# Kernel tuning notes

Measured on AMD Instinct MI355X. Metric: run time of the kernel, lower is better.

Reference implementation:

```python
import jax, jax.numpy as jnp
import numpy as np

B, S, D, H, NS = 4, 2048, 1024, 16, 300
DK = D // H                      # 64
NSP = (NS + H - 1) // H * H      # 304 (padded skills)
DG = NSP // H                    # 19
NEG_FILL = -1e9                  # fp32 path in the torch module


def setup_inputs() -> dict:
    key = jax.random.key(0)
    ks = jax.random.split(key, 12)
    sc = 0.02
    return {
        "context_sequence": jax.random.normal(ks[0], (B, S, D), jnp.float32),
        "value_sequence": jax.random.normal(ks[1], (B, S, NS), jnp.float32),
        "mask": jnp.triu(jnp.ones((S, S), jnp.bool_), k=1),  # causal: True = masked
        # weights stored as [in, out] (math-equivalent to torch's x @ W.T + b)
        "Wq": jax.random.normal(ks[2], (D, D), jnp.float32) * sc,
        "bq": jnp.zeros((D,), jnp.float32),
        "Wk": jax.random.normal(ks[3], (D, D), jnp.float32) * sc,
        "bk": jnp.zeros((D,), jnp.float32),
        "Wv": jax.random.normal(ks[4], (NS, NS), jnp.float32) * sc,
        "bv": jnp.zeros((NS,), jnp.float32),
        "Wg": jax.random.normal(ks[5], (NS, D), jnp.float32) * sc,  # gain_to_context
        "bg": jnp.zeros((D,), jnp.float32),
        "Wo": jax.random.normal(ks[6], (D, D), jnp.float32) * sc,   # output_proj
        "bo": jnp.zeros((D,), jnp.float32),
    }


def reference(context_sequence, value_sequence, mask,
              Wq, bq, Wk, bk, Wv, bv, Wg, bg, Wo, bo):
    b = context_sequence.shape[0]
    orig_dtype = context_sequence.dtype

    # Q, K: [b, H, S, DK]
    Q = (context_sequence @ Wq + bq).reshape(b, -1, H, DK).transpose(0, 2, 1, 3)
    K = (context_sequence @ Wk + bk).reshape(b, -1, H, DK).transpose(0, 2, 1, 3)

    # intrinsic-gain V: project in skill space, zero-pad to NSP, split heads -> [b, H, S, DG]
    V_proj = value_sequence @ Wv + bv
    V_proj = jnp.pad(V_proj, ((0, 0), (0, 0), (0, NSP - NS)))
    V = V_proj.reshape(b, -1, H, DG).transpose(0, 2, 1, 3)

    # fp32 score upcast, scale by sqrt(d_k), mask, cast back, softmax
    scores = jnp.einsum('bhqd,bhkd->bhqk',
                        Q.astype(jnp.float32), K.astype(jnp.float32)) / np.sqrt(DK)
    scores = jnp.where(mask, NEG_FILL, scores).astype(orig_dtype)
    attn = jax.nn.softmax(scores, axis=-1)

    # [b, H, S, DG] -> [b, S, NSP] -> slice to NS
    head_gains = jnp.einsum('bhqk,bhkd->bhqd', attn, V)
    agg = head_gains.transpose(0, 2, 1, 3).reshape(b, -1, NSP)[..., :NS]

    output = agg @ Wg + bg            # gain_to_context
    return output @ Wo + bo           # output_proj (dropout is identity in eval)
```

## Files before the change

### kernel.cpp

```cpp
#include <hip/hip_runtime.h>
#include <math.h>

#define B_   4
#define S_   2048
#define D_   1024
#define H_   16
#define DK_  64
#define NS_  300
#define NSP_ 304
#define DG_  19
#define M_   (B_ * S_)

typedef short bf16x8 __attribute__((ext_vector_type(8)));
typedef short s16x8  __attribute__((ext_vector_type(8)));
typedef short s16x4  __attribute__((ext_vector_type(4)));
typedef float f32x4  __attribute__((ext_vector_type(4)));

__device__ __forceinline__ short f2bf(float f) {
    unsigned u = __float_as_uint(f);
    u += 0x7FFFu + ((u >> 16) & 1u);
    return (short)(u >> 16);
}
__device__ __forceinline__ s16x4 f2bf4(float4 v) {
    s16x4 s; s[0] = f2bf(v.x); s[1] = f2bf(v.y); s[2] = f2bf(v.z); s[3] = f2bf(v.w);
    return s;
}
__device__ __forceinline__ float bf2f(short s) {
    return __uint_as_float(((unsigned)(unsigned short)s) << 16);
}

__device__ __forceinline__ void gload16(const void* g, void* l) {
    __builtin_amdgcn_global_load_lds(
        (const __attribute__((address_space(1))) unsigned int*)g,
        (__attribute__((address_space(3))) unsigned int*)l, 16, 0, 0);
}

__global__ __launch_bounds__(256) void pack_x(const float* __restrict__ src,
                                              short* __restrict__ dst) {
    const int total = M_ * (D_ / 8);
    for (int i = blockIdx.x * 256 + threadIdx.x; i < total; i += gridDim.x * 256) {
        const float4 a = *(const float4*)(src + (size_t)i * 8);
        const float4 b = *(const float4*)(src + (size_t)i * 8 + 4);
        s16x8 o;
        o[0]=f2bf(a.x); o[1]=f2bf(a.y); o[2]=f2bf(a.z); o[3]=f2bf(a.w);
        o[4]=f2bf(b.x); o[5]=f2bf(b.y); o[6]=f2bf(b.z); o[7]=f2bf(b.w);
        *(s16x8*)(dst + (size_t)i * 8) = o;
    }
}

__global__ __launch_bounds__(256) void pack_v(const float* __restrict__ src,
                                              short* __restrict__ dst) {
    const int total = M_ * 75;
    for (int i = blockIdx.x * 256 + threadIdx.x; i < total; i += gridDim.x * 256) {
        const int row = i / 75, c4 = (i - row * 75) * 4;
        const float4 v = *(const float4*)(src + (size_t)row * NS_ + c4);
        *(s16x4*)(dst + (size_t)row * 320 + c4) = f2bf4(v);
    }
}

__global__ __launch_bounds__(256) void transpack_all(
    const float* __restrict__ Wq, const float* __restrict__ Wk,
    const float* __restrict__ Wv, const float* __restrict__ Wo,
    short* __restrict__ WqkT, short* __restrict__ WvT, short* __restrict__ WoT)
{
    __shared__ float tsh[64][65];
    const int z = blockIdx.z, bx = blockIdx.x, by = blockIdx.y;
    const float* src; short* dst; int srs, KR, drs; float scale = 1.f;
    if (z == 0)      { src = Wq; dst = WqkT;              srs = D_;  KR = D_;  drs = D_;  scale = 0.125f; }
    else if (z == 1) { src = Wk; dst = WqkT + 1024 * D_;  srs = D_;  KR = D_;  drs = D_; }
    else if (z == 2) { if (bx >= 5 || by >= 6) return;
                       src = Wv; dst = WvT;               srs = NS_; KR = NS_; drs = 320; }
    else             { src = Wo; dst = WoT;               srs = D_;  KR = D_;  drs = D_; }

    const int k0 = bx * 64, n0 = by * 64;
    const int tt = threadIdx.x;
    const int nx = tt & 63, kyb = tt >> 6;
#pragma unroll
    for (int j = 0; j < 16; ++j) {
        const int k = kyb + j * 4;
        float v = 0.f;
        if (k0 + k < KR && n0 + nx < KR) v = src[(size_t)(k0 + k) * srs + n0 + nx];
        tsh[nx][k] = v;
    }
    __syncthreads();
    const int kx = tt & 63, nyb = tt >> 6;
#pragma unroll
    for (int j = 0; j < 16; ++j) {
        const int n = nyb + j * 4;
        dst[(size_t)(n0 + n) * drs + k0 + kx] = f2bf(tsh[n][kx] * scale);
    }
}

__global__ __launch_bounds__(256) void pack_misc(
    const float* __restrict__ bq, const float* __restrict__ bk, float* __restrict__ bqk,
    short* __restrict__ VpT,
    const float* __restrict__ Wg, short* __restrict__ Wgb)
{
    const int bid = blockIdx.x, t = threadIdx.x;
    if (bid < 8) {
        const int i = bid * 256 + t;
        if (i < 1024) bqk[i] = bq[i] * 0.125f;
        else bqk[i] = bk[i - 1024];
    } else if (bid < 72) {
        const int bh = bid - 8;
        short* row = VpT + ((size_t)bh * 20 + 19) * 2048;
        *(s16x8*)(row + t * 8) = (s16x8)0;
    } else {
        const int i = (bid - 72) * 256 + t;
        const int r = i >> 8, c4 = (i & 255) * 4;
        float4 v = make_float4(0.f, 0.f, 0.f, 0.f);
        if (r < NS_) v = *(const float4*)(Wg + (size_t)r * D_ + c4);
        *(s16x4*)(Wgb + (size_t)r * D_ + c4) = f2bf4(v);
    }
}

__global__ __launch_bounds__(256) void pack_bfused2(const short* __restrict__ WoT,
                                                    const float* __restrict__ bg,
                                                    const float* __restrict__ bo,
                                                    float* __restrict__ dst) {
    __shared__ float part[4];
    const int n = blockIdx.x, t = threadIdx.x;
    const s16x4 w = *(const s16x4*)(WoT + (size_t)n * D_ + t * 4);
    const float4 bgv = *(const float4*)(bg + t * 4);
    float acc = bf2f(w[0]) * bgv.x + bf2f(w[1]) * bgv.y
              + bf2f(w[2]) * bgv.z + bf2f(w[3]) * bgv.w;
#pragma unroll
    for (int m = 1; m < 64; m <<= 1) acc += __shfl_xor(acc, m);
    if ((t & 63) == 0) part[t >> 6] = acc;
    __syncthreads();
    if (t == 0) dst[n] = bo[n] + ((part[0] + part[1]) + (part[2] + part[3]));
}

template<int MODE>
__global__ __launch_bounds__(256) void gemm_k(
    const short* __restrict__ A, int lda,
    const short* __restrict__ Bt, int ldb,
    const float* __restrict__ bias, int blen,
    void* __restrict__ C, int ldc, int nzero, int nstore,
    int K, int gx)
{
    __shared__ __align__(16) short smem[(MODE == 1) ? 17408 : 16384];
    short* As = smem;
    short* Bs = smem + 8192;

    const int nwg = gridDim.x, q = nwg >> 3, fid = blockIdx.x;
    const int wg = (fid & 7) * q + (fid >> 3);
    const int bn = wg % gx, bm = wg / gx;

    const int t = threadIdx.x, l = t & 63, w = t >> 6;
    const int wm = w >> 1, wn = w & 1;
    const int g = l >> 4, c = l & 15;
    const int fsw = (c & 7) << 4;

    const int so  = l * 16;
    const int srow = so >> 7;
    const int skb  = (so & 127) ^ ((srow & 7) << 4);

    f32x4 acc[4][4] = {};
    const size_t ldab = (size_t)lda * 2, ldbb = (size_t)ldb * 2;
    const char* Ab = (const char*)A + (size_t)(bm * 128) * ldab;
    const char* Bb = (const char*)Bt + (size_t)(bn * 128) * ldbb;

    for (int k0 = 0; k0 < K; k0 += 64) {
#pragma unroll
        for (int i = 0; i < 4; ++i) {
            const int chunk = w * 4 + i;
            const int row = chunk * 8 + srow;
            gload16(Ab + (size_t)row * ldab + (size_t)(k0 * 2) + skb,
                    (char*)As + chunk * 1024);
            gload16(Bb + (size_t)row * ldbb + (size_t)(k0 * 2) + skb,
                    (char*)Bs + chunk * 1024);
        }
        __syncthreads();

#pragma unroll
        for (int ks = 0; ks < 2; ++ks) {
            const int kb = (ks * 64 + g * 16) ^ fsw;
            bf16x8 af[4], bf[4];
#pragma unroll
            for (int mt = 0; mt < 4; ++mt)
                af[mt] = *(const bf16x8*)((const char*)As + (wm * 64 + mt * 16 + c) * 128 + kb);
#pragma unroll
            for (int nt = 0; nt < 4; ++nt)
                bf[nt] = *(const bf16x8*)((const char*)Bs + (wn * 64 + nt * 16 + c) * 128 + kb);
            __builtin_amdgcn_s_setprio(1);
#pragma unroll
            for (int mt = 0; mt < 4; ++mt)
#pragma unroll
                for (int nt = 0; nt < 4; ++nt)
                    acc[mt][nt] = __builtin_amdgcn_mfma_f32_16x16x32_bf16(
                        af[mt], bf[nt], acc[mt][nt], 0, 0, 0);
            __builtin_amdgcn_s_setprio(0);
        }
        __syncthreads();
    }

    if (MODE == 1) {
        short* Cs = smem;
#pragma unroll
        for (int mt = 0; mt < 4; ++mt) {
#pragma unroll
            for (int nt = 0; nt < 4; ++nt) {
                const int coll = wn * 64 + nt * 16 + c;
                const int colg = bn * 128 + coll;
                const float bb = (colg < blen) ? bias[colg] : 0.f;
#pragma unroll
                for (int r = 0; r < 4; ++r) {
                    const int rowl = wm * 64 + mt * 16 + 4 * g + r;
                    const short v = (colg < nzero) ? f2bf(acc[mt][nt][r] + bb) : (short)0;
                    Cs[rowl * 136 + coll] = v;
                }
            }
        }
        __syncthreads();
        const int rowl = t >> 1, half = t & 1;
        const int rowg = bm * 128 + rowl;
        short* Cb = (short*)C;
#pragma unroll
        for (int j = 0; j < 8; ++j) {
            const int colg = bn * 128 + half * 64 + j * 8;
            if (colg < nstore)
                *(s16x8*)(Cb + (size_t)rowg * ldc + colg) =
                    *(const s16x8*)(Cs + rowl * 136 + half * 64 + j * 8);
        }
        return;
    }

#pragma unroll
    for (int mt = 0; mt < 4; ++mt) {
#pragma unroll
        for (int nt = 0; nt < 4; ++nt) {
            const int col = bn * 128 + wn * 64 + nt * 16 + c;
            if (MODE == 2) {
                if (col < NSP_) {
                    const int hh = col / DG_, dg = col - hh * DG_;
                    const float bb = (col < blen) ? bias[col] : 0.f;
                    const int m0 = bm * 128 + wm * 64 + mt * 16 + 4 * g;
                    const int bb_ = m0 >> 11, s = m0 & 2047;
                    s16x4 v;
#pragma unroll
                    for (int r = 0; r < 4; ++r) v[r] = f2bf(acc[mt][nt][r] + bb);
                    *(s16x4*)((short*)C + ((size_t)(bb_ * 16 + hh) * 20 + dg) * 2048 + s) = v;
                }
            } else if (col < nstore) {
                const float bb = (col < blen) ? bias[col] : 0.f;
#pragma unroll
                for (int r = 0; r < 4; ++r) {
                    const int row = bm * 128 + wm * 64 + mt * 16 + 4 * g + r;
                    ((float*)C)[(size_t)row * ldc + col] = acc[mt][nt][r] + bb;
                }
            }
        }
    }
}

__global__ __launch_bounds__(256) void attn2(
    const short* __restrict__ QKb, const short* __restrict__ VpT,
    short* __restrict__ aggP)
{
    __shared__ __align__(16) short Qs[64 * 64];
    __shared__ __align__(16) short Ks[128 * 64];
    __shared__ __align__(16) short Vt[32 * 128];
    __shared__ __align__(16) short Pl[4][16 * 128];

    const int fid = blockIdx.x;
    const int wg = (fid & 7) * 256 + (fid >> 3);
    const int b = wg >> 9, h = (wg >> 5) & 15, qt = 31 - (wg & 31);
    const int q0 = qt * 64;

    const int t = threadIdx.x, l = t & 63, w = t >> 6;
    const int g = l >> 4, c = l & 15;
    const int fsw = (c & 7) << 4;

    const char* QKc = (const char*)QKb;
    const char* Vc  = (const char*)VpT + ((size_t)(b * 16 + h) * 20) * 4096;

#pragma unroll
    for (int i = 0; i < 2; ++i) {
        const int chunk = w * 2 + i;
        const int o = chunk * 1024 + l * 16;
        const int row = o >> 7;
        const int kb = (o & 127) ^ ((row & 7) << 4);
        gload16(QKc + (size_t)(b * S_ + q0 + row) * 4096 + h * 128 + kb,
                (char*)Qs + chunk * 1024);
    }
    if (t < 192) *(s16x8*)((char*)Vt + 5120 + t * 16) = (s16x8)0;
    __syncthreads();

    bf16x8 aq[2];
#pragma unroll
    for (int ks = 0; ks < 2; ++ks)
        aq[ks] = *(const bf16x8*)((const char*)Qs + (w * 16 + c) * 128 + ((ks * 64 + g * 16) ^ fsw));

    float l_run[4];
    f32x4 oacc[2] = {};
#pragma unroll
    for (int r = 0; r < 4; ++r) l_run[r] = 0.f;

    const int nkt = (qt >> 1) + 1;
    for (int kt = 0; kt < nkt; ++kt) {
        const int k0 = kt * 128;
#pragma unroll
        for (int i = 0; i < 4; ++i) {
            const int chunk = w * 4 + i;
            const int o = chunk * 1024 + l * 16;
            const int row = o >> 7;
            const int kb = (o & 127) ^ ((row & 7) << 4);
            gload16(QKc + (size_t)(b * S_ + k0 + row) * 4096 + 2048 + h * 128 + kb,
                    (char*)Ks + chunk * 1024);
        }
        for (int i = w; i < 5; i += 4) {
            const int o = i * 1024 + l * 16;
            const int row = o >> 8;
            const int kb = (o & 255) ^ ((row & 7) << 4);
            gload16(Vc + (size_t)row * 4096 + (size_t)(k0 * 2) + kb,
                    (char*)Vt + i * 1024);
        }
        __syncthreads();

        f32x4 st[8] = {};
        __builtin_amdgcn_s_setprio(1);
#pragma unroll
        for (int ks = 0; ks < 2; ++ks) {
            const int kb = (ks * 64 + g * 16) ^ fsw;
#pragma unroll
            for (int nt = 0; nt < 8; ++nt) {
                const bf16x8 bk = *(const bf16x8*)((const char*)Ks + (nt * 16 + c) * 128 + kb);
                st[nt] = __builtin_amdgcn_mfma_f32_16x16x32_bf16(aq[ks], bk, st[nt], 0, 0, 0);
            }
        }
        __builtin_amdgcn_s_setprio(0);

        if (kt == nkt - 1) {
#pragma unroll
            for (int nt = 0; nt < 8; ++nt) {
                const int kvg = k0 + nt * 16 + c;
#pragma unroll
                for (int r = 0; r < 4; ++r) {
                    const int qg = q0 + w * 16 + 4 * g + r;
                    if (kvg > qg) st[nt][r] = -INFINITY;
                }
            }
        }

#pragma unroll
        for (int nt = 0; nt < 8; ++nt)
#pragma unroll
            for (int r = 0; r < 4; ++r)
                st[nt][r] = __expf(st[nt][r]);
#pragma unroll
        for (int r = 0; r < 4; ++r)
            l_run[r] += ((st[0][r] + st[1][r]) + (st[2][r] + st[3][r]))
                      + ((st[4][r] + st[5][r]) + (st[6][r] + st[7][r]));

#pragma unroll
        for (int nt = 0; nt < 8; ++nt)
#pragma unroll
            for (int r = 0; r < 4; ++r)
                Pl[w][(4 * g + r) * 128 + ((nt * 16 + c) ^ (g << 4))] = f2bf(st[nt][r]);

        __builtin_amdgcn_s_setprio(1);
#pragma unroll
        for (int ks = 0; ks < 4; ++ks) {
            const bf16x8 ap = *(const bf16x8*)((const char*)&Pl[w][0] +
                ((c * 256 + ks * 64 + g * 16) ^ (((c >> 2) & 3) << 5)));
            const int kb = (ks * 64 + g * 16) ^ fsw;
#pragma unroll
            for (int nt = 0; nt < 2; ++nt) {
                const bf16x8 bv = *(const bf16x8*)((const char*)Vt + (nt * 16 + c) * 256 + kb);
                oacc[nt] = __builtin_amdgcn_mfma_f32_16x16x32_bf16(ap, bv, oacc[nt], 0, 0, 0);
            }
        }
        __builtin_amdgcn_s_setprio(0);
        __syncthreads();
    }

    float inv[4];
#pragma unroll
    for (int r = 0; r < 4; ++r) {
        float ls = l_run[r];
        ls += __shfl_xor(ls, 1);
        ls += __shfl_xor(ls, 2);
        ls += __shfl_xor(ls, 4);
        ls += __shfl_xor(ls, 8);
        inv[r] = 1.f / ls;
    }
#pragma unroll
    for (int nt = 0; nt < 2; ++nt) {
        const int dg = nt * 16 + c;
        if (dg < DG_) {
#pragma unroll
            for (int r = 0; r < 4; ++r) {
                const int qg = q0 + w * 16 + 4 * g + r;
                aggP[(size_t)(b * S_ + qg) * 320 + h * DG_ + dg] = f2bf(oacc[nt][r] * inv[r]);
            }
        }
    }
}

extern "C" void kernel_launch(void* const* d_in, const int* in_sizes, int n_in,
                              void* d_out, int out_size, void* d_ws, size_t ws_size,
                              hipStream_t stream)
{
    const float* X    = (const float*)d_in[0];
    const float* Vseq = (const float*)d_in[1];
    const float* Wq = (const float*)d_in[3];
    const float* bq = (const float*)d_in[4];
    const float* Wk = (const float*)d_in[5];
    const float* bk = (const float*)d_in[6];
    const float* Wv = (const float*)d_in[7];
    const float* bv = (const float*)d_in[8];
    const float* Wg = (const float*)d_in[9];
    const float* bg = (const float*)d_in[10];
    const float* Wo = (const float*)d_in[11];
    const float* bo = (const float*)d_in[12];
    float* out = (float*)d_out;

    char* p = (char*)d_ws;
    short* Xb    = (short*)p; p += (size_t)M_ * D_ * 2;
    short* QKb   = (short*)p; p += (size_t)M_ * 2048 * 2;
    short* Xv    = (short*)p; p += (size_t)M_ * 320 * 2;
    short* VpT   = (short*)p; p += (size_t)64 * 20 * 2048 * 2;
    short* aggP  = (short*)p; p += (size_t)M_ * 320 * 2;
    short* WqkT  = (short*)p; p += (size_t)2048 * 1024 * 2;
    short* WvT   = (short*)p; p += (size_t)384 * 320 * 2;
    short* Wgb   = (short*)p; p += (size_t)384 * 1024 * 2;
    short* WoT   = (short*)p; p += (size_t)1024 * 1024 * 2;
    short* WgWoT = (short*)p; p += (size_t)1024 * 320 * 2;
    float* bqk   = (float*)p; p += 2048 * 4;
    float* bfus  = (float*)p; p += 1024 * 4;

    pack_x<<<2048, 256, 0, stream>>>(X, Xb);
    pack_v<<<2400, 256, 0, stream>>>(Vseq, Xv);
    transpack_all<<<dim3(16, 16, 4), 256, 0, stream>>>(Wq, Wk, Wv, Wo, WqkT, WvT, WoT);
    pack_misc<<<456, 256, 0, stream>>>(bq, bk, bqk, VpT, Wg, Wgb);
    pack_bfused2<<<D_, 256, 0, stream>>>(WoT, bg, bo, bfus);

    gemm_k<1><<<16 * 64, 256, 0, stream>>>(Xb, D_, WqkT, D_, bqk, 2048,
                                           QKb, 2048, 2048, 2048, D_, 16);
    gemm_k<2><<<3 * 64, 256, 0, stream>>>(Xv, 320, WvT, 320, bv, NS_,
                                          VpT, 0, 0, 0, 320, 3);
    gemm_k<1><<<3 * 8, 256, 0, stream>>>(WoT, D_, Wgb, D_, bfus, 0,
                                         WgWoT, 320, NS_, 320, D_, 3);
    attn2<<<2048, 256, 0, stream>>>(QKb, VpT, aggP);
    gemm_k<0><<<8 * 64, 256, 0, stream>>>(aggP, 320, WgWoT, 320, bfus, D_,
                                          out, D_, D_, D_, 320, 8);
}
```

Baseline: 323.5 us.

## Merge pack and GEMM launches into mega-kernels, stage final GEMM stores through LDS

Folds the five packing kernels into one megapack launch, with the fused bias now computed from the fp32 Wo instead of a separate pass over packed WoT. It also folds the three independent GEMMs into one megagemm launch that branches on block index. The final fp32 GEMM now stages its output tile through LDS for coalesced float4 stores, and the attention P buffer switches from XOR swizzle to a padded row stride. The aim is to cut launch overhead and tail gaps between small kernels and to improve store coalescing, at the cost of heterogeneous blocks sharing one kernel's resources.

After: 300.9 us. -7.0%, faster.

```diff
diff --git a/kernel.cpp b/kernel.cpp
--- a/kernel.cpp
+++ b/kernel.cpp
@@ -25,9 +25,6 @@
     s16x4 s; s[0] = f2bf(v.x); s[1] = f2bf(v.y); s[2] = f2bf(v.z); s[3] = f2bf(v.w);
     return s;
 }
-__device__ __forceinline__ float bf2f(short s) {
-    return __uint_as_float(((unsigned)(unsigned short)s) << 16);
-}
 
 __device__ __forceinline__ void gload16(const void* g, void* l) {
     __builtin_amdgcn_global_load_lds(
@@ -35,116 +32,111 @@
         (__attribute__((address_space(3))) unsigned int*)l, 16, 0, 0);
 }
 
-__global__ __launch_bounds__(256) void pack_x(const float* __restrict__ src,
-                                              short* __restrict__ dst) {
-    const int total = M_ * (D_ / 8);
-    for (int i = blockIdx.x * 256 + threadIdx.x; i < total; i += gridDim.x * 256) {
-        const float4 a = *(const float4*)(src + (size_t)i * 8);
-        const float4 b = *(const float4*)(src + (size_t)i * 8 + 4);
-        s16x8 o;
-        o[0]=f2bf(a.x); o[1]=f2bf(a.y); o[2]=f2bf(a.z); o[3]=f2bf(a.w);
-        o[4]=f2bf(b.x); o[5]=f2bf(b.y); o[6]=f2bf(b.z); o[7]=f2bf(b.w);
-        *(s16x8*)(dst + (size_t)i * 8) = o;
-    }
-}
-
-__global__ __launch_bounds__(256) void pack_v(const float* __restrict__ src,
-                                              short* __restrict__ dst) {
-    const int total = M_ * 75;
-    for (int i = blockIdx.x * 256 + threadIdx.x; i < total; i += gridDim.x * 256) {
-        const int row = i / 75, c4 = (i - row * 75) * 4;
-        const float4 v = *(const float4*)(src + (size_t)row * NS_ + c4);
-        *(s16x4*)(dst + (size_t)row * 320 + c4) = f2bf4(v);
-    }
-}
-
-__global__ __launch_bounds__(256) void transpack_all(
+__global__ __launch_bounds__(256) void megapack(
+    const float* __restrict__ X, const float* __restrict__ Vseq,
     const float* __restrict__ Wq, const float* __restrict__ Wk,
     const float* __restrict__ Wv, const float* __restrict__ Wo,
-    short* __restrict__ WqkT, short* __restrict__ WvT, short* __restrict__ WoT)
-{
-    __shared__ float tsh[64][65];
-    const int z = blockIdx.z, bx = blockIdx.x, by = blockIdx.y;
-    const float* src; short* dst; int srs, KR, drs; float scale = 1.f;
-    if (z == 0)      { src = Wq; dst = WqkT;              srs = D_;  KR = D_;  drs = D_;  scale = 0.125f; }
-    else if (z == 1) { src = Wk; dst = WqkT + 1024 * D_;  srs = D_;  KR = D_;  drs = D_; }
-    else if (z == 2) { if (bx >= 5 || by >= 6) return;
-                       src = Wv; dst = WvT;               srs = NS_; KR = NS_; drs = 320; }
-    else             { src = Wo; dst = WoT;               srs = D_;  KR = D_;  drs = D_; }
-
-    const int k0 = bx * 64, n0 = by * 64;
-    const int tt = threadIdx.x;
-    const int nx = tt & 63, kyb = tt >> 6;
-#pragma unroll
-    for (int j = 0; j < 16; ++j) {
-        const int k = kyb + j * 4;
-        float v = 0.f;
-        if (k0 + k < KR && n0 + nx < KR) v = src[(size_t)(k0 + k) * srs + n0 + nx];
-        tsh[nx][k] = v;
-    }
-    __syncthreads();
-    const int kx = tt & 63, nyb = tt >> 6;
-#pragma unroll
-    for (int j = 0; j < 16; ++j) {
-        const int n = nyb + j * 4;
-        dst[(size_t)(n0 + n) * drs + k0 + kx] = f2bf(tsh[n][kx] * scale);
-    }
-}
-
-__global__ __launch_bounds__(256) void pack_misc(
-    const float* __restrict__ bq, const float* __restrict__ bk, float* __restrict__ bqk,
-    short* __restrict__ VpT,
-    const float* __restrict__ Wg, short* __restrict__ Wgb)
-{
+    const float* __restrict__ Wg,
+    const float* __restrict__ bq, const float* __restrict__ bk,
+    const float* __restrict__ bg, const float* __restrict__ bo,
+    short* __restrict__ Xb, short* __restrict__ Xv,
+    short* __restrict__ WqkT, short* __restrict__ WvT, short* __restrict__ WoT,
+    short* __restrict__ Wgb, short* __restrict__ VpT,
+    float* __restrict__ bqk, float* __restrict__ bfus)
+{
+    __shared__ float shpk[64 * 65];
     const int bid = blockIdx.x, t = threadIdx.x;
-    if (bid < 8) {
-        const int i = bid * 256 + t;
-        if (i < 1024) bqk[i] = bq[i] * 0.125f;
-        else bqk[i] = bk[i - 1024];
-    } else if (bid < 72) {
-        const int bh = bid - 8;
-        short* row = VpT + ((size_t)bh * 20 + 19) * 2048;
-        *(s16x8*)(row + t * 8) = (s16x8)0;
+
+    if (bid < 1024) {
+#pragma unroll
+        for (int j = 0; j < 4; ++j) {
+            const int i = bid * 1024 + j * 256 + t;
+            const float4 a = *(const float4*)(X + (size_t)i * 8);
+            const float4 b = *(const float4*)(X + (size_t)i * 8 + 4);
+            s16x8 o;
+            o[0]=f2bf(a.x); o[1]=f2bf(a.y); o[2]=f2bf(a.z); o[3]=f2bf(a.w);
+            o[4]=f2bf(b.x); o[5]=f2bf(b.y); o[6]=f2bf(b.z); o[7]=f2bf(b.w);
+            *(s16x8*)(Xb + (size_t)i * 8) = o;
+        }
+    } else if (bid < 1624) {
+        const int seg = bid - 1024;
+#pragma unroll
+        for (int j = 0; j < 4; ++j) {
+            const int i = seg * 1024 + j * 256 + t;
+            const int row = i / 75, c4 = (i - row * 75) * 4;
+            const float4 v = *(const float4*)(Vseq + (size_t)row * NS_ + c4);
+            *(s16x4*)(Xv + (size_t)row * 320 + c4) = f2bf4(v);
+        }
+    } else if (bid < 2422) {
+        const int seg = bid - 1624;
+        const float* src; short* dst; int srs, R, drs, bx, by; float scale = 1.f;
+        if (seg < 256)      { src = Wq; dst = WqkT;             srs = D_;  R = D_;  drs = D_;  scale = 0.125f; bx = seg & 15; by = seg >> 4; }
+        else if (seg < 512) { src = Wk; dst = WqkT + 1024 * D_; srs = D_;  R = D_;  drs = D_;  bx = (seg-256) & 15; by = (seg-256) >> 4; }
+        else if (seg < 542) { src = Wv; dst = WvT;              srs = NS_; R = NS_; drs = 320; bx = (seg-512) % 5;  by = (seg-512) / 5; }
+        else                { src = Wo; dst = WoT;              srs = D_;  R = D_;  drs = D_;  bx = (seg-542) & 15; by = (seg-542) >> 4; }
+        const int k0 = bx * 64, n0 = by * 64;
+        const int nx = t & 63, kyb = t >> 6;
+#pragma unroll
+        for (int j = 0; j < 16; ++j) {
+            const int k = kyb + j * 4;
+            float v = 0.f;
+            if (k0 + k < R && n0 + nx < R) v = src[(size_t)(k0 + k) * srs + n0 + nx];
+            shpk[nx * 65 + k] = v;
+        }
+        __syncthreads();
+        const int kx = t & 63, nyb = t >> 6;
+#pragma unroll
+        for (int j = 0; j < 16; ++j) {
+            const int n = nyb + j * 4;
+            dst[(size_t)(n0 + n) * drs + k0 + kx] = f2bf(shpk[n * 65 + kx] * scale);
+        }
+    } else if (bid < 2878) {
+        const int seg = bid - 2422;
+        if (seg < 8) {
+            const int i = seg * 256 + t;
+            if (i < 1024) bqk[i] = bq[i] * 0.125f;
+            else bqk[i] = bk[i - 1024];
+        } else if (seg < 72) {
+            const int bh = seg - 8;
+            short* row = VpT + ((size_t)bh * 20 + 19) * 2048;
+            *(s16x8*)(row + t * 8) = (s16x8)0;
+        } else {
+            const int i = (seg - 72) * 256 + t;
+            const int r = i >> 8, c4 = (i & 255) * 4;
+            float4 v = make_float4(0.f, 0.f, 0.f, 0.f);
+            if (r < NS_) v = *(const float4*)(Wg + (size_t)r * D_ + c4);
+            *(s16x4*)(Wgb + (size_t)r * D_ + c4) = f2bf4(v);
+        }
     } else {
-        const int i = (bid - 72) * 256 + t;
-        const int r = i >> 8, c4 = (i & 255) * 4;
-        float4 v = make_float4(0.f, 0.f, 0.f, 0.f);
-        if (r < NS_) v = *(const float4*)(Wg + (size_t)r * D_ + c4);
-        *(s16x4*)(Wgb + (size_t)r * D_ + c4) = f2bf4(v);
-    }
-}
-
-__global__ __launch_bounds__(256) void pack_bfused2(const short* __restrict__ WoT,
-                                                    const float* __restrict__ bg,
-                                                    const float* __restrict__ bo,
-                                                    float* __restrict__ dst) {
-    __shared__ float part[4];
-    const int n = blockIdx.x, t = threadIdx.x;
-    const s16x4 w = *(const s16x4*)(WoT + (size_t)n * D_ + t * 4);
-    const float4 bgv = *(const float4*)(bg + t * 4);
-    float acc = bf2f(w[0]) * bgv.x + bf2f(w[1]) * bgv.y
-              + bf2f(w[2]) * bgv.z + bf2f(w[3]) * bgv.w;
-#pragma unroll
-    for (int m = 1; m < 64; m <<= 1) acc += __shfl_xor(acc, m);
-    if ((t & 63) == 0) part[t >> 6] = acc;
-    __syncthreads();
-    if (t == 0) dst[n] = bo[n] + ((part[0] + part[1]) + (part[2] + part[3]));
+        const int n0 = (bid - 2878) * 64;
+        const int dt = t >> 6, cn = t & 63;
+        float acc = 0.f;
+        for (int dd = 0; dd < 256; ++dd) {
+            const int d = dd * 4 + dt;
+            acc += bg[d] * Wo[(size_t)d * D_ + n0 + cn];
+        }
+        shpk[dt * 64 + cn] = acc;
+        __syncthreads();
+        if (t < 64)
+            bfus[n0 + t] = bo[n0 + t] +
+                ((shpk[t] + shpk[64 + t]) + (shpk[128 + t] + shpk[192 + t]));
+    }
 }
 
 template<int MODE>
-__global__ __launch_bounds__(256) void gemm_k(
+__device__ __forceinline__ void gemm_body(
+    int bid, int nwg,
     const short* __restrict__ A, int lda,
     const short* __restrict__ Bt, int ldb,
     const float* __restrict__ bias, int blen,
     void* __restrict__ C, int ldc, int nzero, int nstore,
-    int K, int gx)
-{
-    __shared__ __align__(16) short smem[(MODE == 1) ? 17408 : 16384];
+    int K, int gx, short* smem)
+{
     short* As = smem;
     short* Bs = smem + 8192;
 
-    const int nwg = gridDim.x, q = nwg >> 3, fid = blockIdx.x;
-    const int wg = (fid & 7) * q + (fid >> 3);
+    const int q = nwg >> 3;
+    const int wg = (bid & 7) * q + (bid >> 3);
     const int bn = wg % gx, bm = wg / gx;
 
     const int t = threadIdx.x, l = t & 63, w = t >> 6;
@@ -195,6 +187,37 @@
         __syncthreads();
     }
 
+    if (MODE == 0) {
+        float* Csf = (float*)smem;
+#pragma unroll
+        for (int hh = 0; hh < 2; ++hh) {
+            if (wm == hh) {
+#pragma unroll
+                for (int mt = 0; mt < 4; ++mt)
+#pragma unroll
+                    for (int nt = 0; nt < 4; ++nt) {
+                        const int coll = wn * 64 + nt * 16 + c;
+                        const int colg = bn * 128 + coll;
+                        const float bb = (colg < blen) ? bias[colg] : 0.f;
+#pragma unroll
+                        for (int r = 0; r < 4; ++r)
+                            Csf[(mt * 16 + 4 * g + r) * 132 + coll] = acc[mt][nt][r] + bb;
+                    }
+            }
+            __syncthreads();
+            const int rowl = t >> 2, c4 = t & 3;
+            const int rowg = bm * 128 + hh * 64 + rowl;
+            float* Cf = (float*)C + (size_t)rowg * ldc + bn * 128;
+#pragma unroll
+            for (int j = 0; j < 8; ++j) {
+                const int cf = (c4 + j * 4) * 4;
+                *(float4*)(Cf + cf) = *(const float4*)(Csf + rowl * 132 + cf);
+            }
+            __syncthreads();
+        }
+        return;
+    }
+
     if (MODE == 1) {
         short* Cs = smem;
 #pragma unroll
@@ -231,27 +254,48 @@
 #pragma unroll
         for (int nt = 0; nt < 4; ++nt) {
             const int col = bn * 128 + wn * 64 + nt * 16 + c;
-            if (MODE == 2) {
-                if (col < NSP_) {
-                    const int hh = col / DG_, dg = col - hh * DG_;
-                    const float bb = (col < blen) ? bias[col] : 0.f;
-                    const int m0 = bm * 128 + wm * 64 + mt * 16 + 4 * g;
-                    const int bb_ = m0 >> 11, s = m0 & 2047;
-                    s16x4 v;
-#pragma unroll
-                    for (int r = 0; r < 4; ++r) v[r] = f2bf(acc[mt][nt][r] + bb);
-                    *(s16x4*)((short*)C + ((size_t)(bb_ * 16 + hh) * 20 + dg) * 2048 + s) = v;
-                }
-            } else if (col < nstore) {
+            if (col < NSP_) {
+                const int hh = col / DG_, dg = col - hh * DG_;
                 const float bb = (col < blen) ? bias[col] : 0.f;
-#pragma unroll
-                for (int r = 0; r < 4; ++r) {
-                    const int row = bm * 128 + wm * 64 + mt * 16 + 4 * g + r;
-                    ((float*)C)[(size_t)row * ldc + col] = acc[mt][nt][r] + bb;
-                }
-            }
-        }
-    }
+                const int m0 = bm * 128 + wm * 64 + mt * 16 + 4 * g;
+                const int bb_ = m0 >> 11, s = m0 & 2047;
+                s16x4 v;
+#pragma unroll
+                for (int r = 0; r < 4; ++r) v[r] = f2bf(acc[mt][nt][r] + bb);
+                *(s16x4*)((short*)C + ((size_t)(bb_ * 16 + hh) * 20 + dg) * 2048 + s) = v;
+            }
+        }
+    }
+}
+
+__global__ __launch_bounds__(256) void megagemm(
+    const short* __restrict__ Xb, const short* __restrict__ WqkT,
+    const float* __restrict__ bqk, short* __restrict__ QKb,
+    const short* __restrict__ Xv, const short* __restrict__ WvT,
+    const float* __restrict__ bv, short* __restrict__ VpT,
+    const short* __restrict__ WoT, const short* __restrict__ Wgb,
+    short* __restrict__ WgWoT)
+{
+    __shared__ __align__(16) short smem[17408];
+    const int bid = blockIdx.x;
+    if (bid < 1024)
+        gemm_body<1>(bid, 1024, Xb, D_, WqkT, D_, bqk, 2048,
+                     QKb, 2048, 2048, 2048, D_, 16, smem);
+    else if (bid < 1216)
+        gemm_body<2>(bid - 1024, 192, Xv, 320, WvT, 320, bv, NS_,
+                     VpT, 0, 0, 0, 320, 3, smem);
+    else
+        gemm_body<1>(bid - 1216, 24, WoT, D_, Wgb, D_, (const float*)nullptr, 0,
+                     WgWoT, 320, NS_, 320, D_, 3, smem);
+}
+
+__global__ __launch_bounds__(256) void gemm_final(
+    const short* __restrict__ aggP, const short* __restrict__ WgWoT,
+    const float* __restrict__ bfus, float* __restrict__ out)
+{
+    __shared__ __align__(16) short smem[17408];
+    gemm_body<0>(blockIdx.x, 512, aggP, 320, WgWoT, 320, bfus, D_,
+                 out, D_, D_, D_, 320, 8, smem);
 }
 
 __global__ __launch_bounds__(256) void attn2(
@@ -261,7 +305,7 @@
     __shared__ __align__(16) short Qs[64 * 64];
     __shared__ __align__(16) short Ks[128 * 64];
     __shared__ __align__(16) short Vt[32 * 128];
-    __shared__ __align__(16) short Pl[4][16 * 128];
+    __shared__ __align__(16) short Pl[4][16 * 136];
 
     const int fid = blockIdx.x;
     const int wg = (fid & 7) * 256 + (fid >> 3);
@@ -357,13 +401,12 @@
         for (int nt = 0; nt < 8; ++nt)
 #pragma unroll
             for (int r = 0; r < 4; ++r)
-                Pl[w][(4 * g + r) * 128 + ((nt * 16 + c) ^ (g << 4))] = f2bf(st[nt][r]);
+                Pl[w][(4 * g + r) * 136 + nt * 16 + c] = f2bf(st[nt][r]);
 
         __builtin_amdgcn_s_setprio(1);
 #pragma unroll
         for (int ks = 0; ks < 4; ++ks) {
-            const bf16x8 ap = *(const bf16x8*)((const char*)&Pl[w][0] +
-                ((c * 256 + ks * 64 + g * 16) ^ (((c >> 2) & 3) << 5)));
+            const bf16x8 ap = *(const bf16x8*)((const char*)&Pl[w][0] + c * 272 + ks * 64 + g * 16);
             const int kb = (ks * 64 + g * 16) ^ fsw;
 #pragma unroll
             for (int nt = 0; nt < 2; ++nt) {
@@ -430,19 +473,13 @@
     float* bqk   = (float*)p; p += 2048 * 4;
     float* bfus  = (float*)p; p += 1024 * 4;
 
-    pack_x<<<2048, 256, 0, stream>>>(X, Xb);
-    pack_v<<<2400, 256, 0, stream>>>(Vseq, Xv);
-    transpack_all<<<dim3(16, 16, 4), 256, 0, stream>>>(Wq, Wk, Wv, Wo, WqkT, WvT, WoT);
-    pack_misc<<<456, 256, 0, stream>>>(bq, bk, bqk, VpT, Wg, Wgb);
-    pack_bfused2<<<D_, 256, 0, stream>>>(WoT, bg, bo, bfus);
-
-    gemm_k<1><<<16 * 64, 256, 0, stream>>>(Xb, D_, WqkT, D_, bqk, 2048,
-                                           QKb, 2048, 2048, 2048, D_, 16);
-    gemm_k<2><<<3 * 64, 256, 0, stream>>>(Xv, 320, WvT, 320, bv, NS_,
-                                          VpT, 0, 0, 0, 320, 3);
-    gemm_k<1><<<3 * 8, 256, 0, stream>>>(WoT, D_, Wgb, D_, bfus, 0,
-                                         WgWoT, 320, NS_, 320, D_, 3);
+    megapack<<<2894, 256, 0, stream>>>(X, Vseq, Wq, Wk, Wv, Wo, Wg,
+                                       bq, bk, bg, bo,
+                                       Xb, Xv, WqkT, WvT, WoT, Wgb, VpT,
+                                       bqk, bfus);
+    megagemm<<<1240, 256, 0, stream>>>(Xb, WqkT, bqk, QKb,
+                                       Xv, WvT, bv, VpT,
+                                       WoT, Wgb, WgWoT);
     attn2<<<2048, 256, 0, stream>>>(QKb, VpT, aggP);
-    gemm_k<0><<<8 * 64, 256, 0, stream>>>(aggP, 320, WgWoT, 320, bfus, D_,
-                                          out, D_, D_, D_, 320, 8);
-}
+    gemm_final<<<512, 256, 0, stream>>>(aggP, WgWoT, bfus, out);
+}
```
